# Kernel tuning notes

Measured on AMD Instinct MI355X. Metric: run time of the kernel, lower is better.

Reference implementation:

```python
import jax, jax.numpy as jnp
import numpy as np

B, C, H, W = 4, 256, 64, 64
CQK = C // 8  # 32


def setup_inputs() -> dict:
    key = jax.random.key(0)
    ks = jax.random.split(key, 8)
    s = 0.05
    return {
        "x": jax.random.normal(ks[0], (B, C, H, W), dtype=jnp.float32),
        "wq": jax.random.normal(ks[1], (CQK, C), dtype=jnp.float32) * s,
        "bq": jax.random.normal(ks[2], (CQK,), dtype=jnp.float32) * s,
        "wk": jax.random.normal(ks[3], (CQK, C), dtype=jnp.float32) * s,
        "bk": jax.random.normal(ks[4], (CQK,), dtype=jnp.float32) * s,
        "wv": jax.random.normal(ks[5], (C, C), dtype=jnp.float32) * s,
        "bv": jax.random.normal(ks[6], (C,), dtype=jnp.float32) * s,
        "gamma": jax.random.normal(ks[7], (1,), dtype=jnp.float32),
    }


def reference(x, wq, bq, wk, bk, wv, bv, gamma):
    b, c, h, w = x.shape
    n = h * w
    xf = x.reshape(b, c, n)  # (B, C, N)
    # 1x1 conv + bias + ReLU (Conv2d wrapper default activate='relu')
    q = jax.nn.relu(jnp.einsum('oc,bcn->bon', wq, xf) + bq[:, None])  # (B, CQK, N)
    k = jax.nn.relu(jnp.einsum('oc,bcn->bon', wk, xf) + bk[:, None])  # (B, CQK, N)
    v = jax.nn.relu(jnp.einsum('oc,bcn->bon', wv, xf) + bv[:, None])  # (B, C, N)
    # energy[b, i, j] = sum_c q[b, c, i] * k[b, c, j]
    energy = jnp.einsum('bci,bcj->bij', q, k)  # (B, N, N)
    attention = jax.nn.softmax(energy, axis=-1)
    # out[b, c, i] = sum_j v[b, c, j] * attention[b, i, j]
    out = jnp.einsum('bcj,bij->bci', v, attention)  # (B, C, N)
    out = out.reshape(b, c, h, w)
    return gamma[0] * out + x
```

## Files before the change

kernel.cpp:

```cpp
#include <hip/hip_runtime.h>
#include <stdint.h>


#define NB 4
#define CD 256
#define ND 4096
#define CQ 32
#define LOG2E 1.4426950408889634f

typedef __attribute__((ext_vector_type(4))) float f32x4;
typedef __attribute__((ext_vector_type(8))) _Float16 f16x8;
typedef __attribute__((ext_vector_type(4))) unsigned short u16x4;
typedef __attribute__((ext_vector_type(8))) unsigned short u16x8;
typedef __attribute__((ext_vector_type(2))) unsigned int u32x2;
typedef __attribute__((ext_vector_type(4))) int i32x4;

static __device__ __forceinline__ unsigned short f2h(float f) {
    union { _Float16 h; unsigned short u; } cv; cv.h = (_Float16)f; return cv.u;
}
static __device__ __forceinline__ float fexp2(float xv) {
    float r; asm("v_exp_f32 %0, %1" : "=v"(r) : "v"(xv)); return r;
}

#define BARRIER() asm volatile("s_waitcnt lgkmcnt(0)\n\ts_barrier" ::: "memory")

__global__ __launch_bounds__(256) void cvt_kernel(
    const float* __restrict__ x,
    const float* __restrict__ wq, const float* __restrict__ wk,
    const float* __restrict__ wv,
    unsigned short* __restrict__ xh, unsigned short* __restrict__ Wh)
{
    __shared__ unsigned short xt[64 * 72];
    if (blockIdx.x >= 1024) {
        const int idx = (blockIdx.x - 1024) * 256 + threadIdx.x;
        const int m = idx >> 6, kq = (idx & 63) << 2;
        const float* src = (m < 32) ? (wq + (size_t)m * CD + kq)
                         : (m < 64) ? (wk + (size_t)(m - 32) * CD + kq)
                                    : (wv + (size_t)(m - 64) * CD + kq);
        const f32x4 v = *reinterpret_cast<const f32x4*>(src);
        u16x4 h;
#pragma unroll
        for (int u = 0; u < 4; ++u) h[u] = f2h(v[u]);
        *reinterpret_cast<u16x4*>(Wh + (size_t)m * CD + kq) = h;
        return;
    }
    const int t  = threadIdx.x;
    const int nt = blockIdx.x & 63, ct = (blockIdx.x >> 6) & 3, b = blockIdx.x >> 8;
    const int n0 = nt << 6, c0 = ct << 6;

    const float* xb = x + ((size_t)(b * CD + c0)) * ND + n0;
#pragma unroll
    for (int s = t; s < 1024; s += 256) {
        const int c = s >> 4, nq = (s & 15) << 2;
        const f32x4 v = *reinterpret_cast<const f32x4*>(xb + (size_t)c * ND + nq);
        u16x4 h;
#pragma unroll
        for (int u = 0; u < 4; ++u) h[u] = f2h(v[u]);
        *reinterpret_cast<u16x4*>(&xt[c * 72 + nq]) = h;
    }
    __syncthreads();

    const int n = t >> 2, cb = (t & 3) << 4;
    u16x8 o0, o1;
#pragma unroll
    for (int u = 0; u < 8; ++u) o0[u] = xt[(cb + u) * 72 + n];
#pragma unroll
    for (int u = 0; u < 8; ++u) o1[u] = xt[(cb + 8 + u) * 72 + n];
    unsigned short* dst = xh + ((size_t)(b * ND + n0 + n)) * CD + c0 + cb;
    *reinterpret_cast<u16x8*>(dst)     = o0;
    *reinterpret_cast<u16x8*>(dst + 8) = o1;
}

__global__ __launch_bounds__(320) void proj_kernel(
    const unsigned short* __restrict__ Wh, const unsigned short* __restrict__ xh,
    const float* __restrict__ bq, const float* __restrict__ bk,
    const float* __restrict__ bv,
    unsigned short* __restrict__ Qt, unsigned short* __restrict__ Kt,
    unsigned short* __restrict__ Vp)
{
    const int tid = threadIdx.x;
    const int lane = tid & 63;
    const int w = __builtin_amdgcn_readfirstlane(tid >> 6);
    const int m16 = lane & 15, g4 = lane >> 4;
    const int b = blockIdx.x >> 6, n0 = (blockIdx.x & 63) << 6;

    f32x4 acc[4][4];
#pragma unroll
    for (int a = 0; a < 4; ++a)
#pragma unroll
        for (int c = 0; c < 4; ++c) acc[a][c] = (f32x4){0.f, 0.f, 0.f, 0.f};

    const unsigned short* Wrow = Wh + (size_t)(w * 64 + m16) * CD;
    const unsigned short* Xrow = xh + ((size_t)(b * ND + n0 + m16)) * CD;

#pragma unroll
    for (int ks = 0; ks < 8; ++ks) {
        const int ko = ks * 32 + g4 * 8;
        f16x8 af[4], bf[4];
#pragma unroll
        for (int ms = 0; ms < 4; ++ms)
            af[ms] = *reinterpret_cast<const f16x8*>(Wrow + (size_t)ms * 16 * CD + ko);
#pragma unroll
        for (int ns = 0; ns < 4; ++ns)
            bf[ns] = *reinterpret_cast<const f16x8*>(Xrow + (size_t)ns * 16 * CD + ko);
        if (w == 0) {
#pragma unroll
            for (int ms = 0; ms < 4; ++ms)
#pragma unroll
                for (int ns = 0; ns < 4; ++ns)
                    acc[ms][ns] = __builtin_amdgcn_mfma_f32_16x16x32_f16(
                        af[ms], bf[ns], acc[ms][ns], 0, 0, 0);
        } else {
#pragma unroll
            for (int ms = 0; ms < 4; ++ms)
#pragma unroll
                for (int ns = 0; ns < 4; ++ns)
                    acc[ms][ns] = __builtin_amdgcn_mfma_f32_16x16x32_f16(
                        bf[ns], af[ms], acc[ms][ns], 0, 0, 0);
        }
    }

    if (w == 0) {
#pragma unroll
        for (int ms = 0; ms < 4; ++ms) {
            const int seg = ms * 16;
            const int mb  = seg + g4 * 4;
            const f32x4 bias = (seg < 32) ? *reinterpret_cast<const f32x4*>(bq + mb)
                                          : *reinterpret_cast<const f32x4*>(bk + (mb - 32));
#pragma unroll
            for (int ns = 0; ns < 4; ++ns) {
                const int n = n0 + ns * 16 + m16;
                u16x4 h;
                if (seg < 32) {
#pragma unroll
                    for (int r = 0; r < 4; ++r)
                        h[r] = f2h(fmaxf(acc[ms][ns][r] + bias[r], 0.f) * LOG2E);
                    *reinterpret_cast<u16x4*>(Qt + ((size_t)(b * ND + n)) * CQ + mb) = h;
                } else {
#pragma unroll
                    for (int r = 0; r < 4; ++r)
                        h[r] = f2h(fmaxf(acc[ms][ns][r] + bias[r], 0.f));
                    *reinterpret_cast<u16x4*>(Kt + ((size_t)(b * ND + n)) * CQ + (mb - 32)) = h;
                }
            }
        }
    } else {
        const int cbase = (w - 1) * 64;
#pragma unroll
        for (int ms = 0; ms < 4; ++ms) {
            const int c = cbase + ms * 16 + m16;
            const float bval = bv[c];
#pragma unroll
            for (int ns = 0; ns < 4; ++ns) {
                const int n = n0 + ns * 16 + g4 * 4;
                u16x4 h;
#pragma unroll
                for (int r = 0; r < 4; ++r)
                    h[r] = f2h(fmaxf(acc[ms][ns][r] + bval, 0.f));
                unsigned short* dst = Vp
                    + ((size_t)((b * 128 + (n >> 5)) * 16 + (c >> 4))) * 512
                    + ((((n >> 3) & 3) * 16 + (c & 15)) * 8) + (n & 7);
                *reinterpret_cast<u16x4*>(dst) = h;
            }
        }
    }
}

__global__ __launch_bounds__(512, 2) void attn_kernel(
    const unsigned short* __restrict__ Qt, const unsigned short* __restrict__ Kt,
    const unsigned short* __restrict__ Vp, const float* __restrict__ x,
    const float* __restrict__ gamma, float* __restrict__ out)
{
    __shared__ __align__(16) unsigned char smem[68096];
    float* scales = reinterpret_cast<float*>(smem + 32768);
    int*   flags  = reinterpret_cast<int*>(smem + 34816);
    float* Ocomb  = reinterpret_cast<float*>(smem);
    float* mfin   = reinterpret_cast<float*>(smem + 66560);
    float* lfin   = reinterpret_cast<float*>(smem + 67072);
    float* wfac   = reinterpret_cast<float*>(smem + 67584);

    const int tid  = threadIdx.x;
    const int lane = tid & 63;
    const int w8   = __builtin_amdgcn_readfirstlane(tid >> 6);
    const int g    = w8 >> 2;
    const int ws   = w8 & 3;
    const int m16  = lane & 15;
    const int g4   = lane >> 4;
    const int wg   = (blockIdx.x & 7) * 32 + (blockIdx.x >> 3);
    const int b    = wg >> 6;
    const int i0   = (wg & 63) << 6;

    const f16x8 qfrag = *reinterpret_cast<const f16x8*>(
        Qt + ((size_t)(b * ND + i0 + ws * 16 + m16)) * CQ + g4 * 8);
    const unsigned short* kb = Kt + ((size_t)(b * ND + m16)) * CQ + g4 * 8;
    const unsigned short* vpc =
        Vp + ((size_t)(b * 128 * 16 + ws * 4)) * 512 + lane * 8;

    f32x4 oacc[4][4];
#pragma unroll
    for (int a = 0; a < 4; ++a)
#pragma unroll
        for (int c = 0; c < 4; ++c) oacc[a][c] = (f32x4){0.f, 0.f, 0.f, 0.f};
    float mrow = -1e30f, lrow = 0.f;
    const f32x4 zero4 = {0.f, 0.f, 0.f, 0.f};

    const int jbase = g * 2048;
    const int irow  = ws * 16 + m16;
    const int iswz  = (m16 & 7) << 4;

    auto LOADK = [&](f16x8 (&kr)[4], int j) {
#pragma unroll
        for (int t = 0; t < 4; ++t)
            kr[t] = *reinterpret_cast<const f16x8*>(kb + (size_t)(j + t * 16) * CQ);
    };

    auto STEP = [&](int k, f16x8 (&kc)[4], f16x8 (&kn)[4]) {
        const int j0  = jbase + k * 64;
        const int par = k & 1;
        unsigned char* pb = smem + g * 16384 + par * 8192;

        const int jblk0 = j0 >> 5;
        f16x8 vf[2][4];
#pragma unroll
        for (int jh = 0; jh < 2; ++jh)
#pragma unroll
            for (int cs = 0; cs < 4; ++cs)
                vf[jh][cs] = *reinterpret_cast<const f16x8*>(
                    vpc + (size_t)((jblk0 + jh) * 16 + cs) * 512);
        const int jn = (k < 31) ? (j0 + 64) : jbase;
        LOADK(kn, jn);

        f32x4 s[4];
#pragma unroll
        for (int t = 0; t < 4; ++t)
            s[t] = __builtin_amdgcn_mfma_f32_16x16x32_f16(kc[t], qfrag, zero4, 0, 0, 0);

        float pm = s[0][0];
#pragma unroll
        for (int t = 0; t < 4; ++t)
#pragma unroll
            for (int r = 0; r < 4; ++r) pm = fmaxf(pm, s[t][r]);
        pm = fmaxf(pm, __shfl_xor(pm, 16));
        pm = fmaxf(pm, __shfl_xor(pm, 32));
        float sc = 1.0f;
        int myresc = 0;
        if (__ballot(pm <= mrow + 8.0f) != ~0ull) {
            const float mnew = fmaxf(mrow, pm);
            sc = fexp2(mrow - mnew);
            mrow = mnew;
            myresc = 1;
        }
        float rs = 0.f;
#pragma unroll
        for (int t = 0; t < 4; ++t)
#pragma unroll
            for (int r = 0; r < 4; ++r) { s[t][r] = fexp2(s[t][r] - mrow); rs += s[t][r]; }
        rs += __shfl_xor(rs, 16);
        rs += __shfl_xor(rs, 32);
        lrow = lrow * sc + rs;

#pragma unroll
        for (int t = 0; t < 4; ++t) {
            u32x2 pw;
            pw[0] = __builtin_bit_cast(unsigned int,
                        __builtin_amdgcn_cvt_pkrtz(s[t][0], s[t][1]));
            pw[1] = __builtin_bit_cast(unsigned int,
                        __builtin_amdgcn_cvt_pkrtz(s[t][2], s[t][3]));
            const int lo = (irow * 128 + t * 32 + g4 * 8) ^ iswz;
            *reinterpret_cast<u32x2*>(pb + lo) = pw;
        }
        if (g4 == 0)   scales[(g * 2 + par) * 64 + irow] = sc;
        if (lane == 0) flags[(g * 2 + par) * 4 + ws] = myresc;

        BARRIER();

        const i32x4 fl = *reinterpret_cast<const i32x4*>(flags + (g * 2 + par) * 4);
        const int anyresc = __builtin_amdgcn_readfirstlane(fl[0] | fl[1] | fl[2] | fl[3]);
        if (anyresc) {
#pragma unroll
            for (int is = 0; is < 4; ++is) {
                const f32x4 sr = *reinterpret_cast<const f32x4*>(
                    scales + (g * 2 + par) * 64 + is * 16 + g4 * 4);
#pragma unroll
                for (int r = 0; r < 4; ++r)
#pragma unroll
                    for (int cs = 0; cs < 4; ++cs) oacc[is][cs][r] *= sr[r];
            }
        }

        __builtin_amdgcn_s_setprio(1);
#pragma unroll
        for (int jh = 0; jh < 2; ++jh) {
#pragma unroll
            for (int is = 0; is < 4; ++is) {
                const int lo = ((is * 16 + m16) * 128 + jh * 64 + g4 * 16) ^ iswz;
                const f16x8 pf = *reinterpret_cast<const f16x8*>(pb + lo);
#pragma unroll
                for (int cs = 0; cs < 4; ++cs)
                    oacc[is][cs] = __builtin_amdgcn_mfma_f32_16x16x32_f16(
                        pf, vf[jh][cs], oacc[is][cs], 0, 0, 0);
            }
        }
        __builtin_amdgcn_s_setprio(0);
    };

    f16x8 kA[4], kB[4];
    LOADK(kA, jbase);

#pragma unroll 1
    for (int k2 = 0; k2 < 16; ++k2) {
        STEP(2 * k2,     kA, kB);
        STEP(2 * k2 + 1, kB, kA);
    }

    if (g4 == 0) { mfin[g * 64 + irow] = mrow; lfin[g * 64 + irow] = lrow; }
    __syncthreads();

    if (tid < 128) {
        const int gg = tid >> 6, i = tid & 63;
        const float m0 = mfin[i], m1 = mfin[64 + i];
        const float M  = fmaxf(m0, m1);
        const float e0 = fexp2(m0 - M), e1 = fexp2(m1 - M);
        const float den = lfin[i] * e0 + lfin[64 + i] * e1;
        wfac[tid] = ((gg == 0) ? e0 : e1) / den;
    }
    __syncthreads();

    if (g == 0) {
#pragma unroll
        for (int is = 0; is < 4; ++is) {
            const f32x4 f = *reinterpret_cast<const f32x4*>(wfac + is * 16 + g4 * 4);
#pragma unroll
            for (int cs = 0; cs < 4; ++cs)
#pragma unroll
                for (int r = 0; r < 4; ++r)
                    Ocomb[(is * 16 + g4 * 4 + r) * 260 + ws * 64 + cs * 16 + m16] =
                        oacc[is][cs][r] * f[r];
        }
    }
    __syncthreads();
    if (g == 1) {
#pragma unroll
        for (int is = 0; is < 4; ++is) {
            const f32x4 f = *reinterpret_cast<const f32x4*>(wfac + 64 + is * 16 + g4 * 4);
#pragma unroll
            for (int cs = 0; cs < 4; ++cs)
#pragma unroll
                for (int r = 0; r < 4; ++r)
                    Ocomb[(is * 16 + g4 * 4 + r) * 260 + ws * 64 + cs * 16 + m16] +=
                        oacc[is][cs][r] * f[r];
        }
    }
    __syncthreads();

    const float gm = gamma[0];
#pragma unroll
    for (int pass = 0; pass < 8; ++pass) {
        const int c  = (tid >> 4) + pass * 32;
        const int ib = (tid & 15) * 4;
        f32x4 o;
#pragma unroll
        for (int u = 0; u < 4; ++u) o[u] = Ocomb[(ib + u) * 260 + c];
        const size_t idx = ((size_t)(b * CD + c)) * ND + i0 + ib;
        const f32x4 xv = *reinterpret_cast<const f32x4*>(x + idx);
        f32x4 res;
#pragma unroll
        for (int u = 0; u < 4; ++u) res[u] = gm * o[u] + xv[u];
        *reinterpret_cast<f32x4*>(out + idx) = res;
    }
}

extern "C" void kernel_launch(void* const* d_in, const int* in_sizes, int n_in,
                              void* d_out, int out_size, void* d_ws, size_t ws_size,
                              hipStream_t stream) {
    const float* x     = (const float*)d_in[0];
    const float* wq    = (const float*)d_in[1];
    const float* bq    = (const float*)d_in[2];
    const float* wk    = (const float*)d_in[3];
    const float* bk    = (const float*)d_in[4];
    const float* wv    = (const float*)d_in[5];
    const float* bv    = (const float*)d_in[6];
    const float* gamma = (const float*)d_in[7];

    unsigned short* Qt = (unsigned short*)d_ws;
    unsigned short* Kt = Qt + (size_t)NB * ND * CQ;
    unsigned short* Vp = Kt + (size_t)NB * ND * CQ;
    unsigned short* Wh = Vp + (size_t)NB * CD * ND;
    unsigned short* xh = Wh + (size_t)320 * CD;
    float* out = (float*)d_out;

    cvt_kernel<<<dim3(1104),     dim3(256), 0, stream>>>(x, wq, wk, wv, xh, Wh);
    proj_kernel<<<dim3(NB * 64), dim3(320), 0, stream>>>(Wh, xh, bq, bk, bv, Qt, Kt, Vp);
    attn_kernel<<<dim3(NB * 64), dim3(512), 0, stream>>>(Qt, Kt, Vp, x, gamma, out);
}
```

Baseline: 78.02 us.

## Split attention key range across four wave groups with 1024-thread blocks

Attention blocks grow from 512 to 1024 threads, and the key dimension is split four ways (1024 keys per group) instead of two. Partial softmax statistics and outputs from the four groups are merged through shared memory in a serialized four-step accumulation. The goal is more waves per CU to hide latency, since the grid has only 256 blocks on a device with many CUs. The cost is more serialized merge passes and barriers, more shared memory, and register pressure from the waves_per_eu setting.

```diff
diff --git a/kernel.cpp b/kernel.cpp
--- a/kernel.cpp
+++ b/kernel.cpp
@@ -166,24 +166,25 @@
     }
 }
 
-__global__ __launch_bounds__(512, 2) void attn_kernel(
+__global__ __launch_bounds__(1024) __attribute__((amdgpu_waves_per_eu(4, 4)))
+void attn_kernel(
     const unsigned short* __restrict__ Qt, const unsigned short* __restrict__ Kt,
     const unsigned short* __restrict__ Vp, const float* __restrict__ x,
     const float* __restrict__ gamma, float* __restrict__ out)
 {
-    __shared__ __align__(16) unsigned char smem[68096];
-    float* scales = reinterpret_cast<float*>(smem + 32768);
-    int*   flags  = reinterpret_cast<int*>(smem + 34816);
+    __shared__ __align__(16) unsigned char smem[70784];
+    float* scales = reinterpret_cast<float*>(smem + 65536);
+    int*   flags  = reinterpret_cast<int*>(smem + 67584);
     float* Ocomb  = reinterpret_cast<float*>(smem);
-    float* mfin   = reinterpret_cast<float*>(smem + 66560);
-    float* lfin   = reinterpret_cast<float*>(smem + 67072);
-    float* wfac   = reinterpret_cast<float*>(smem + 67584);
+    float* mfin   = reinterpret_cast<float*>(smem + 67712);
+    float* lfin   = reinterpret_cast<float*>(smem + 68736);
+    float* wfac   = reinterpret_cast<float*>(smem + 69760);
 
     const int tid  = threadIdx.x;
     const int lane = tid & 63;
-    const int w8   = __builtin_amdgcn_readfirstlane(tid >> 6);
-    const int g    = w8 >> 2;
-    const int ws   = w8 & 3;
+    const int w16  = __builtin_amdgcn_readfirstlane(tid >> 6);
+    const int g    = w16 >> 2;
+    const int ws   = w16 & 3;
     const int m16  = lane & 15;
     const int g4   = lane >> 4;
     const int wg   = (blockIdx.x & 7) * 32 + (blockIdx.x >> 3);
@@ -204,7 +205,7 @@
     float mrow = -1e30f, lrow = 0.f;
     const f32x4 zero4 = {0.f, 0.f, 0.f, 0.f};
 
-    const int jbase = g * 2048;
+    const int jbase = g * 1024;
     const int irow  = ws * 16 + m16;
     const int iswz  = (m16 & 7) << 4;
 
@@ -227,7 +228,7 @@
             for (int cs = 0; cs < 4; ++cs)
                 vf[jh][cs] = *reinterpret_cast<const f16x8*>(
                     vpc + (size_t)((jblk0 + jh) * 16 + cs) * 512);
-        const int jn = (k < 31) ? (j0 + 64) : jbase;
+        const int jn = (k < 15) ? (j0 + 64) : jbase;
         LOADK(kn, jn);
 
         f32x4 s[4];
@@ -308,7 +309,7 @@
     LOADK(kA, jbase);
 
 #pragma unroll 1
-    for (int k2 = 0; k2 < 16; ++k2) {
+    for (int k2 = 0; k2 < 8; ++k2) {
         STEP(2 * k2,     kA, kB);
         STEP(2 * k2 + 1, kB, kA);
     }
@@ -316,48 +317,46 @@
     if (g4 == 0) { mfin[g * 64 + irow] = mrow; lfin[g * 64 + irow] = lrow; }
     __syncthreads();
 
-    if (tid < 128) {
+    if (tid < 256) {
         const int gg = tid >> 6, i = tid & 63;
-        const float m0 = mfin[i], m1 = mfin[64 + i];
-        const float M  = fmaxf(m0, m1);
-        const float e0 = fexp2(m0 - M), e1 = fexp2(m1 - M);
-        const float den = lfin[i] * e0 + lfin[64 + i] * e1;
-        wfac[tid] = ((gg == 0) ? e0 : e1) / den;
+        const float m0 = mfin[i], m1 = mfin[64 + i], m2 = mfin[128 + i], m3 = mfin[192 + i];
+        const float M  = fmaxf(fmaxf(m0, m1), fmaxf(m2, m3));
+        const float e0 = fexp2(m0 - M), e1 = fexp2(m1 - M),
+                    e2 = fexp2(m2 - M), e3 = fexp2(m3 - M);
+        const float den = lfin[i] * e0 + lfin[64 + i] * e1 +
+                          lfin[128 + i] * e2 + lfin[192 + i] * e3;
+        const float eg = (gg == 0) ? e0 : (gg == 1) ? e1 : (gg == 2) ? e2 : e3;
+        wfac[gg * 64 + i] = eg / den;
     }
     __syncthreads();
 
-    if (g == 0) {
-#pragma unroll
-        for (int is = 0; is < 4; ++is) {
-            const f32x4 f = *reinterpret_cast<const f32x4*>(wfac + is * 16 + g4 * 4);
-#pragma unroll
-            for (int cs = 0; cs < 4; ++cs)
-#pragma unroll
-                for (int r = 0; r < 4; ++r)
-                    Ocomb[(is * 16 + g4 * 4 + r) * 260 + ws * 64 + cs * 16 + m16] =
-                        oacc[is][cs][r] * f[r];
-        }
-    }
-    __syncthreads();
-    if (g == 1) {
-#pragma unroll
-        for (int is = 0; is < 4; ++is) {
-            const f32x4 f = *reinterpret_cast<const f32x4*>(wfac + 64 + is * 16 + g4 * 4);
-#pragma unroll
-            for (int cs = 0; cs < 4; ++cs)
-#pragma unroll
-                for (int r = 0; r < 4; ++r)
-                    Ocomb[(is * 16 + g4 * 4 + r) * 260 + ws * 64 + cs * 16 + m16] +=
-                        oacc[is][cs][r] * f[r];
-        }
-    }
-    __syncthreads();
+#pragma unroll
+    for (int gg = 0; gg < 4; ++gg) {
+        if (g == gg) {
+#pragma unroll
+            for (int is = 0; is < 4; ++is) {
+                const f32x4 f = *reinterpret_cast<const f32x4*>(
+                    wfac + g * 64 + is * 16 + g4 * 4);
+#pragma unroll
+                for (int cs = 0; cs < 4; ++cs)
+#pragma unroll
+                    for (int r = 0; r < 4; ++r) {
+                        const int i = is * 16 + g4 * 4 + r;
+                        const int c = ws * 64 + cs * 16 + m16;
+                        if (gg == 0) Ocomb[i * 260 + c]  = oacc[is][cs][r] * f[r];
+                        else         Ocomb[i * 260 + c] += oacc[is][cs][r] * f[r];
+                    }
+            }
+        }
+        __syncthreads();
+    }
 
     const float gm = gamma[0];
 #pragma unroll
-    for (int pass = 0; pass < 8; ++pass) {
-        const int c  = (tid >> 4) + pass * 32;
-        const int ib = (tid & 15) * 4;
+    for (int pass = 0; pass < 4; ++pass) {
+        const int q  = tid + pass * 1024;
+        const int c  = q >> 4;
+        const int ib = (q & 15) * 4;
         f32x4 o;
 #pragma unroll
         for (int u = 0; u < 4; ++u) o[u] = Ocomb[(ib + u) * 260 + c];
@@ -389,7 +388,7 @@
     unsigned short* xh = Wh + (size_t)320 * CD;
     float* out = (float*)d_out;
 
-    cvt_kernel<<<dim3(1104),     dim3(256), 0, stream>>>(x, wq, wk, wv, xh, Wh);
-    proj_kernel<<<dim3(NB * 64), dim3(320), 0, stream>>>(Wh, xh, bq, bk, bv, Qt, Kt, Vp);
-    attn_kernel<<<dim3(NB * 64), dim3(512), 0, stream>>>(Qt, Kt, Vp, x, gamma, out);
-}
+    cvt_kernel<<<dim3(1104),     dim3(256),  0, stream>>>(x, wq, wk, wv, xh, Wh);
+    proj_kernel<<<dim3(NB * 64), dim3(320),  0, stream>>>(Wh, xh, bq, bk, bv, Qt, Kt, Vp);
+    attn_kernel<<<dim3(NB * 64), dim3(1024), 0, stream>>>(Qt, Kt, Vp, x, gamma, out);
+}
```

Result: slower. 242.3 us (+210.6%).

## Process 128 keys per attention step and defer row-sum reductions

Applied to the files above, without the earlier changes.

Doubles the key tile handled per softmax/PV step from 64 to 128. That halves the number of barriers and loop iterations, and the per-step P buffers in shared memory grow to match. The cross-lane row-max shuffle now runs only when a rescale is needed, and the row-sum shuffle is moved out of the loop to a single reduction at the end. In exchange, register demand rises a lot (8 K fragments double-buffered, 8 score tiles, an extra set of V fragments) under 512-thread, 2-block launch bounds, which risks spills or lower occupancy. The scales and flags arrays are also relocated in shared memory.

```diff
diff --git a/kernel.cpp b/kernel.cpp
--- a/kernel.cpp
+++ b/kernel.cpp
@@ -172,8 +172,8 @@
     const float* __restrict__ gamma, float* __restrict__ out)
 {
     __shared__ __align__(16) unsigned char smem[68096];
-    float* scales = reinterpret_cast<float*>(smem + 32768);
-    int*   flags  = reinterpret_cast<int*>(smem + 34816);
+    float* scales = reinterpret_cast<float*>(smem + 65536);
+    int*   flags  = reinterpret_cast<int*>(smem + 67584);
     float* Ocomb  = reinterpret_cast<float*>(smem);
     float* mfin   = reinterpret_cast<float*>(smem + 66560);
     float* lfin   = reinterpret_cast<float*>(smem + 67072);
@@ -201,23 +201,24 @@
     for (int a = 0; a < 4; ++a)
 #pragma unroll
         for (int c = 0; c < 4; ++c) oacc[a][c] = (f32x4){0.f, 0.f, 0.f, 0.f};
-    float mrow = -1e30f, lrow = 0.f;
+    float mrow = -1e30f;
+    float lrow = 0.f;
     const f32x4 zero4 = {0.f, 0.f, 0.f, 0.f};
 
     const int jbase = g * 2048;
     const int irow  = ws * 16 + m16;
     const int iswz  = (m16 & 7) << 4;
 
-    auto LOADK = [&](f16x8 (&kr)[4], int j) {
-#pragma unroll
-        for (int t = 0; t < 4; ++t)
+    auto LOADK = [&](f16x8 (&kr)[8], int j) {
+#pragma unroll
+        for (int t = 0; t < 8; ++t)
             kr[t] = *reinterpret_cast<const f16x8*>(kb + (size_t)(j + t * 16) * CQ);
     };
 
-    auto STEP = [&](int k, f16x8 (&kc)[4], f16x8 (&kn)[4]) {
-        const int j0  = jbase + k * 64;
+    auto STEP = [&](int k, f16x8 (&kc)[8], f16x8 (&kn)[8]) {
+        const int j0  = jbase + k * 128;
         const int par = k & 1;
-        unsigned char* pb = smem + g * 16384 + par * 8192;
+        unsigned char* pb = smem + g * 32768 + par * 16384;
 
         const int jblk0 = j0 >> 5;
         f16x8 vf[2][4];
@@ -227,50 +228,57 @@
             for (int cs = 0; cs < 4; ++cs)
                 vf[jh][cs] = *reinterpret_cast<const f16x8*>(
                     vpc + (size_t)((jblk0 + jh) * 16 + cs) * 512);
-        const int jn = (k < 31) ? (j0 + 64) : jbase;
+        const int jn = (k < 15) ? (j0 + 128) : jbase;
         LOADK(kn, jn);
 
-        f32x4 s[4];
-#pragma unroll
-        for (int t = 0; t < 4; ++t)
+        f32x4 s[8];
+#pragma unroll
+        for (int t = 0; t < 8; ++t)
             s[t] = __builtin_amdgcn_mfma_f32_16x16x32_f16(kc[t], qfrag, zero4, 0, 0, 0);
 
         float pm = s[0][0];
 #pragma unroll
-        for (int t = 0; t < 4; ++t)
+        for (int t = 0; t < 8; ++t)
 #pragma unroll
             for (int r = 0; r < 4; ++r) pm = fmaxf(pm, s[t][r]);
-        pm = fmaxf(pm, __shfl_xor(pm, 16));
-        pm = fmaxf(pm, __shfl_xor(pm, 32));
         float sc = 1.0f;
         int myresc = 0;
         if (__ballot(pm <= mrow + 8.0f) != ~0ull) {
-            const float mnew = fmaxf(mrow, pm);
+            float pr = pm;
+            pr = fmaxf(pr, __shfl_xor(pr, 16));
+            pr = fmaxf(pr, __shfl_xor(pr, 32));
+            const float mnew = fmaxf(mrow, pr);
             sc = fexp2(mrow - mnew);
             mrow = mnew;
             myresc = 1;
         }
         float rs = 0.f;
 #pragma unroll
-        for (int t = 0; t < 4; ++t)
+        for (int t = 0; t < 8; ++t)
 #pragma unroll
             for (int r = 0; r < 4; ++r) { s[t][r] = fexp2(s[t][r] - mrow); rs += s[t][r]; }
-        rs += __shfl_xor(rs, 16);
-        rs += __shfl_xor(rs, 32);
         lrow = lrow * sc + rs;
 
 #pragma unroll
-        for (int t = 0; t < 4; ++t) {
+        for (int t = 0; t < 8; ++t) {
             u32x2 pw;
             pw[0] = __builtin_bit_cast(unsigned int,
                         __builtin_amdgcn_cvt_pkrtz(s[t][0], s[t][1]));
             pw[1] = __builtin_bit_cast(unsigned int,
                         __builtin_amdgcn_cvt_pkrtz(s[t][2], s[t][3]));
-            const int lo = (irow * 128 + t * 32 + g4 * 8) ^ iswz;
+            const int lo = (irow * 256 + t * 32 + g4 * 8) ^ iswz;
             *reinterpret_cast<u32x2*>(pb + lo) = pw;
         }
         if (g4 == 0)   scales[(g * 2 + par) * 64 + irow] = sc;
         if (lane == 0) flags[(g * 2 + par) * 4 + ws] = myresc;
+
+        f16x8 vf2[2][4];
+#pragma unroll
+        for (int jh = 0; jh < 2; ++jh)
+#pragma unroll
+            for (int cs = 0; cs < 4; ++cs)
+                vf2[jh][cs] = *reinterpret_cast<const f16x8*>(
+                    vpc + (size_t)((jblk0 + 2 + jh) * 16 + cs) * 512);
 
         BARRIER();
 
@@ -290,29 +298,36 @@
 
         __builtin_amdgcn_s_setprio(1);
 #pragma unroll
-        for (int jh = 0; jh < 2; ++jh) {
+        for (int jh = 0; jh < 4; ++jh) {
 #pragma unroll
             for (int is = 0; is < 4; ++is) {
-                const int lo = ((is * 16 + m16) * 128 + jh * 64 + g4 * 16) ^ iswz;
+                const int lo = ((is * 16 + m16) * 256 + jh * 64 + g4 * 16) ^ iswz;
                 const f16x8 pf = *reinterpret_cast<const f16x8*>(pb + lo);
-#pragma unroll
-                for (int cs = 0; cs < 4; ++cs)
+                const f16x8 vv = (jh < 2) ? vf[jh][0] : vf2[jh - 2][0];
+#pragma unroll
+                for (int cs = 0; cs < 4; ++cs) {
+                    const f16x8 vb = (jh == 0) ? vf[0][cs] : (jh == 1) ? vf[1][cs]
+                                   : (jh == 2) ? vf2[0][cs] : vf2[1][cs];
                     oacc[is][cs] = __builtin_amdgcn_mfma_f32_16x16x32_f16(
-                        pf, vf[jh][cs], oacc[is][cs], 0, 0, 0);
+                        pf, vb, oacc[is][cs], 0, 0, 0);
+                }
+                (void)vv;
             }
         }
         __builtin_amdgcn_s_setprio(0);
     };
 
-    f16x8 kA[4], kB[4];
+    f16x8 kA[8], kB[8];
     LOADK(kA, jbase);
 
 #pragma unroll 1
-    for (int k2 = 0; k2 < 16; ++k2) {
+    for (int k2 = 0; k2 < 8; ++k2) {
         STEP(2 * k2,     kA, kB);
         STEP(2 * k2 + 1, kB, kA);
     }
 
+    lrow += __shfl_xor(lrow, 16);
+    lrow += __shfl_xor(lrow, 32);
     if (g4 == 0) { mfin[g * 64 + irow] = mrow; lfin[g * 64 + irow] = lrow; }
     __syncthreads();
 
@@ -322,7 +337,7 @@
         const float M  = fmaxf(m0, m1);
         const float e0 = fexp2(m0 - M), e1 = fexp2(m1 - M);
         const float den = lfin[i] * e0 + lfin[64 + i] * e1;
-        wfac[tid] = ((gg == 0) ? e0 : e1) / den;
+        wfac[gg * 64 + i] = ((gg == 0) ? e0 : e1) / den;
     }
     __syncthreads();
 
```

Result: slower. 94.65 us (+21.3%).

## Replace block barrier with per-group LDS counter sync and defer row shuffles

Applied to the files above, without the earlier changes.

The full-workgroup s_barrier in each attention step is replaced by a spin-wait on a shared-memory atomic counter per 4-wave group. The two key-range groups no longer have to wait for each other. Separately, the cross-lane max reduction now runs only when a rescale is triggered, and the row-sum shuffle reduction moves out of the loop to after it. The trade-off is spin polling with s_sleep and LDS atomics in place of the hardware barrier, which may cost more latency than it saves.

```diff
diff --git a/kernel.cpp b/kernel.cpp
--- a/kernel.cpp
+++ b/kernel.cpp
@@ -21,8 +21,6 @@
 static __device__ __forceinline__ float fexp2(float xv) {
     float r; asm("v_exp_f32 %0, %1" : "=v"(r) : "v"(xv)); return r;
 }
-
-#define BARRIER() asm volatile("s_waitcnt lgkmcnt(0)\n\ts_barrier" ::: "memory")
 
 __global__ __launch_bounds__(256) void cvt_kernel(
     const float* __restrict__ x,
@@ -172,6 +170,7 @@
     const float* __restrict__ gamma, float* __restrict__ out)
 {
     __shared__ __align__(16) unsigned char smem[68096];
+    __shared__ int gctr[2];
     float* scales = reinterpret_cast<float*>(smem + 32768);
     int*   flags  = reinterpret_cast<int*>(smem + 34816);
     float* Ocomb  = reinterpret_cast<float*>(smem);
@@ -190,6 +189,9 @@
     const int b    = wg >> 6;
     const int i0   = (wg & 63) << 6;
 
+    if (tid < 2) gctr[tid] = 0;
+    __syncthreads();
+
     const f16x8 qfrag = *reinterpret_cast<const f16x8*>(
         Qt + ((size_t)(b * ND + i0 + ws * 16 + m16)) * CQ + g4 * 8);
     const unsigned short* kb = Kt + ((size_t)(b * ND + m16)) * CQ + g4 * 8;
@@ -201,7 +203,8 @@
     for (int a = 0; a < 4; ++a)
 #pragma unroll
         for (int c = 0; c < 4; ++c) oacc[a][c] = (f32x4){0.f, 0.f, 0.f, 0.f};
-    float mrow = -1e30f, lrow = 0.f;
+    float mrow = -1e30f;
+    float lrow = 0.f;
     const f32x4 zero4 = {0.f, 0.f, 0.f, 0.f};
 
     const int jbase = g * 2048;
@@ -212,6 +215,17 @@
 #pragma unroll
         for (int t = 0; t < 4; ++t)
             kr[t] = *reinterpret_cast<const f16x8*>(kb + (size_t)(j + t * 16) * CQ);
+    };
+
+    auto GSYNC = [&](int k) {
+        asm volatile("s_waitcnt lgkmcnt(0)" ::: "memory");
+        if (lane == 0) atomicAdd(&gctr[g], 1);
+        const int tgt = (k + 1) * 4;
+        int cv;
+        do {
+            __builtin_amdgcn_s_sleep(1);
+            cv = __builtin_amdgcn_readfirstlane(*(volatile int*)&gctr[g]);
+        } while (cv < tgt);
     };
 
     auto STEP = [&](int k, f16x8 (&kc)[4], f16x8 (&kn)[4]) {
@@ -240,12 +254,12 @@
         for (int t = 0; t < 4; ++t)
 #pragma unroll
             for (int r = 0; r < 4; ++r) pm = fmaxf(pm, s[t][r]);
-        pm = fmaxf(pm, __shfl_xor(pm, 16));
-        pm = fmaxf(pm, __shfl_xor(pm, 32));
         float sc = 1.0f;
         int myresc = 0;
         if (__ballot(pm <= mrow + 8.0f) != ~0ull) {
-            const float mnew = fmaxf(mrow, pm);
+            float pr = fmaxf(pm, __shfl_xor(pm, 16));
+            pr = fmaxf(pr, __shfl_xor(pr, 32));
+            const float mnew = fmaxf(mrow, pr);
             sc = fexp2(mrow - mnew);
             mrow = mnew;
             myresc = 1;
@@ -255,8 +269,6 @@
         for (int t = 0; t < 4; ++t)
 #pragma unroll
             for (int r = 0; r < 4; ++r) { s[t][r] = fexp2(s[t][r] - mrow); rs += s[t][r]; }
-        rs += __shfl_xor(rs, 16);
-        rs += __shfl_xor(rs, 32);
         lrow = lrow * sc + rs;
 
 #pragma unroll
@@ -272,7 +284,7 @@
         if (g4 == 0)   scales[(g * 2 + par) * 64 + irow] = sc;
         if (lane == 0) flags[(g * 2 + par) * 4 + ws] = myresc;
 
-        BARRIER();
+        GSYNC(k);
 
         const i32x4 fl = *reinterpret_cast<const i32x4*>(flags + (g * 2 + par) * 4);
         const int anyresc = __builtin_amdgcn_readfirstlane(fl[0] | fl[1] | fl[2] | fl[3]);
@@ -313,6 +325,8 @@
         STEP(2 * k2 + 1, kB, kA);
     }
 
+    lrow += __shfl_xor(lrow, 16);
+    lrow += __shfl_xor(lrow, 32);
     if (g4 == 0) { mfin[g * 64 + irow] = mrow; lfin[g * 64 + irow] = lrow; }
     __syncthreads();
 
@@ -322,7 +336,7 @@
         const float M  = fmaxf(m0, m1);
         const float e0 = fexp2(m0 - M), e1 = fexp2(m1 - M);
         const float den = lfin[i] * e0 + lfin[64 + i] * e1;
-        wfac[tid] = ((gg == 0) ? e0 : e1) / den;
+        wfac[gg * 64 + i] = ((gg == 0) ? e0 : e1) / den;
     }
     __syncthreads();
 
```

Result: faster. 71.71 us (-8.1%).
